# Optimization experiments

Hardware: AMD Instinct MI355X
Metric: run time of the kernel (lower is better)

Reference implementation:

```python
import jax, jax.numpy as jnp
import numpy as np
import math

G = 8        # groups
ORDER = 2    # Taylor order
GAMMA = 1e-4 # RBF gamma
EPS = 1e-5   # GroupNorm eps


def setup_inputs() -> dict:
    key = jax.random.key(0)
    ks = jax.random.split(key, 6)
    B, C_HI, C_LO, P = 16, 512, 512, 256
    H1 = W1 = 64
    H2 = W2 = 32
    s = 0.02
    return {
        "input_high": jax.random.normal(ks[0], (B, C_HI, H1, W1), jnp.float32),
        "input_low": jax.random.normal(ks[1], (B, C_LO, H2, W2), jnp.float32),
        "Wt": jax.random.normal(ks[2], (P, C_HI), jnp.float32) * s,
        "Wp": jax.random.normal(ks[3], (P, C_LO), jnp.float32) * s,
        "Wg": jax.random.normal(ks[4], (P, C_LO), jnp.float32) * s,
        # grouped 1x1 conv planes -> inplanes1: [G, out_per_group, in_per_group]
        "Wz": jax.random.normal(ks[5], (G, C_HI // G, P // G), jnp.float32) * s,
        "gn_w": jnp.ones((C_HI,), jnp.float32),
        "gn_b": jnp.zeros((C_HI,), jnp.float32),
    }


def _taylor_alpha():
    # alpha_k = sqrt((2*gamma)^k / k! * exp(-2*gamma)) for k = 0..ORDER
    ks = np.arange(ORDER + 1)
    fact = np.array([math.factorial(int(k)) for k in ks], dtype=np.float64)
    a = np.sqrt((2.0 * GAMMA) ** ks / fact * np.exp(-2.0 * GAMMA))
    return jnp.asarray(a, jnp.float32)


def reference(input_high, input_low, Wt, Wp, Wg, Wz, gn_w, gn_b):
    # 1x1-conv projections as channel contractions
    t = jnp.einsum('bchw,oc->bohw', input_high, Wt)   # [b, P, h1, w1]
    p = jnp.einsum('bchw,oc->bohw', input_low, Wp)    # [b, P, h2, w2]
    g = jnp.einsum('bchw,oc->bohw', input_low, Wg)    # [b, P, h2, w2]
    b, c1, h1, w1 = t.shape

    alpha = _taylor_alpha()                            # [ORDER+1]
    # split channels into groups, flatten (c/G)*h*w per group
    tg = t.reshape(b, G, -1)                           # [b, G, N1]
    pg = p.reshape(b, G, -1)                           # [b, G, N2]
    gg = g.reshape(b, G, -1)                           # [b, G, N2]

    # low-rank Taylor feature maps: [b, G, ORDER+1, N]
    t_tay = jnp.stack([tg ** k for k in range(ORDER + 1)], axis=2) * alpha[None, None, :, None]
    p_tay = jnp.stack([pg ** k for k in range(ORDER + 1)], axis=2) * alpha[None, None, :, None]

    att = jnp.einsum('bgkn,bgn->bgk', p_tay, gg)       # [b, G, ORDER+1]
    x = jnp.einsum('bgk,bgkn->bgn', att, t_tay)        # [b, G, N1]
    x = x.reshape(b, G, c1 // G, h1, w1)               # grouped feature map

    # grouped 1x1 conv z: planes -> inplanes1
    z = jnp.einsum('bgihw,goi->bgohw', x, Wz)
    z = z.reshape(b, -1, h1, w1)                       # [b, C_HI, h1, w1]

    # GroupNorm(num_groups=G) with affine, then residual
    zg = z.reshape(b, G, -1)
    mu = zg.mean(axis=-1, keepdims=True)
    var = zg.var(axis=-1, keepdims=True)
    zn = ((zg - mu) * jax.lax.rsqrt(var + EPS)).reshape(z.shape)
    out = zn * gn_w[None, :, None, None] + gn_b[None, :, None, None] + input_high
    return out
```

## Files before the change

kernel.cpp:

```cpp
#include <hip/hip_runtime.h>
#include <math.h>

typedef __attribute__((ext_vector_type(8))) short short8;
typedef __attribute__((ext_vector_type(8))) unsigned short u16x8;
typedef __attribute__((ext_vector_type(4))) float f32x4;

#define EPS_ 1e-5f

__device__ inline unsigned int cvtpk(float a, float b) {
    unsigned int r;
    asm("v_cvt_pk_bf16_f32 %0, %1, %2" : "=v"(r) : "v"(a), "v"(b));
    return r;
}

__device__ inline f32x4 mfma16(u16x8 a, u16x8 b, f32x4 c) {
    return __builtin_amdgcn_mfma_f32_16x16x32_bf16((short8)a, (short8)b, c, 0, 0, 0);
}

__global__ __launch_bounds__(256)
void k0s(const float* __restrict__ xlo, float* __restrict__ sxsum)
{
    __shared__ float sred[256];
    int blk = blockIdx.x;
    int cgrp = blk & 15, b = blk >> 4;
    int tid = threadIdx.x;
    int cl = tid >> 3, seg = tid & 7;
    int c = cgrp * 32 + cl;
    const float* row = xlo + ((size_t)b * 512 + c) * 1024 + seg * 128;
    float s = 0.f;
#pragma unroll
    for (int i = 0; i < 32; i++) {
        float4 v = ((const float4*)row)[i];
        s += v.x + v.y + v.z + v.w;
    }
    sred[tid] = s;
    __syncthreads();
    if (seg == 0) {
        float t = 0.f;
#pragma unroll
        for (int e = 0; e < 8; e++) t += sred[cl * 8 + e];
        sxsum[(size_t)b * 512 + c] = t;
    }
}

#define K1_BODY(C0, VCUR, VNXT, DOPREF)                                          \
  {                                                                              \
    if (DOPREF) {                                                                \
        const float* xc = xlo + ((size_t)b * 512 + (C0) + 64 + cs * 8) * 1024 + hw0 + xrow; \
        _Pragma("unroll")                                                        \
        for (int j = 0; j < 8; j++) VNXT[j] = xc[(size_t)j * 1024];              \
    }                                                                            \
    __syncthreads();                                                             \
    _Pragma("unroll")                                                            \
    for (int k = 0; k < 4; k++) {                                                \
        int idx = k * 256 + tid;                                                 \
        int row = idx >> 3, s = idx & 7;                                         \
        const float* pp = Wp + (size_t)(pbase + row) * 512 + (C0) + s * 8;       \
        const float* pg = Wg + (size_t)(pbase + row) * 512 + (C0) + s * 8;       \
        float4 a0 = ((const float4*)pp)[0], a1 = ((const float4*)pp)[1];         \
        float4 b0 = ((const float4*)pg)[0], b1 = ((const float4*)pg)[1];         \
        uint4 qp = { cvtpk(a0.x,a0.y), cvtpk(a0.z,a0.w),                         \
                     cvtpk(a1.x,a1.y), cvtpk(a1.z,a1.w) };                       \
        uint4 qg = { cvtpk(b0.x,b0.y), cvtpk(b0.z,b0.w),                         \
                     cvtpk(b1.x,b1.y), cvtpk(b1.z,b1.w) };                       \
        int off = row * 64 + ((s ^ (row & 7)) << 3);                             \
        *(uint4*)&sWp[off] = qp;                                                 \
        *(uint4*)&sWg[off] = qg;                                                 \
    }                                                                            \
    {                                                                            \
        uint4 q = { cvtpk(VCUR[0],VCUR[1]), cvtpk(VCUR[2],VCUR[3]),              \
                    cvtpk(VCUR[4],VCUR[5]), cvtpk(VCUR[6],VCUR[7]) };            \
        int phys = cs ^ (xrow & 7);                                              \
        *(uint4*)&sX1[xrow * 64 + phys * 8] = q;                                 \
    }                                                                            \
    __syncthreads();                                                             \
    _Pragma("unroll")                                                            \
    for (int kk = 0; kk < 2; kk++) {                                             \
        u16x8 bf[2];                                                             \
        _Pragma("unroll")                                                        \
        for (int ht = 0; ht < 2; ht++) {                                         \
            int row = ht * 16 + l15;                                             \
            bf[ht] = *(const u16x8*)&sX1[row * 64 + (((kk*4+l4) ^ (row&7)) << 3)]; \
        }                                                                        \
        _Pragma("unroll")                                                        \
        for (int i = 0; i < 2; i++) {                                            \
            int row = w * 32 + i * 16 + l15;                                     \
            int off = row * 64 + (((kk*4+l4) ^ (row&7)) << 3);                   \
            u16x8 ap = *(const u16x8*)&sWp[off];                                 \
            u16x8 ag = *(const u16x8*)&sWg[off];                                 \
            _Pragma("unroll")                                                    \
            for (int ht = 0; ht < 2; ht++) {                                     \
                pacc[i][ht] = mfma16(ap, bf[ht], pacc[i][ht]);                   \
                gacc[i][ht] = mfma16(ag, bf[ht], gacc[i][ht]);                   \
            }                                                                    \
        }                                                                        \
    }                                                                            \
  }

__global__ __launch_bounds__(256, 4)
void k1_att(const float* __restrict__ xlo, const float* __restrict__ Wp,
            const float* __restrict__ Wg, float* __restrict__ att_part)
{
    __shared__ unsigned short sWp[8192];
    __shared__ unsigned short sWg[8192];
    __shared__ unsigned short sX1[2048];

    int tid = threadIdx.x;
    int w = tid >> 6, lane = tid & 63;
    int l15 = lane & 15, l4 = lane >> 4;
    int beta = blockIdx.x;
    int tile = beta & 31, mh = (beta >> 5) & 1, b = beta >> 6;
    int hw0 = tile * 32;
    int pbase = mh * 128;
    int xrow = tid & 31, cs = tid >> 5;

    f32x4 pacc[2][2] = {};
    f32x4 gacc[2][2] = {};

    float vbA[8], vbB[8];
    {
        const float* xc = xlo + ((size_t)b * 512 + cs * 8) * 1024 + hw0 + xrow;
#pragma unroll
        for (int j = 0; j < 8; j++) vbA[j] = xc[(size_t)j * 1024];
    }

    for (int kc2 = 0; kc2 < 4; kc2++) {
        int c0 = kc2 * 128;
        K1_BODY(c0,      vbA, vbB, true);
        K1_BODY(c0 + 64, vbB, vbA, (kc2 < 3));
    }

    float s1 = 0.f, s2 = 0.f;
#pragma unroll
    for (int i = 0; i < 2; i++)
#pragma unroll
        for (int ht = 0; ht < 2; ht++)
#pragma unroll
            for (int r = 0; r < 4; r++) {
                float pv = pacc[i][ht][r], gv = gacc[i][ht][r];
                s1 += pv * gv; s2 += pv * pv * gv;
            }
#pragma unroll
    for (int m = 1; m < 64; m <<= 1) {
        s1 += __shfl_xor(s1, m);
        s2 += __shfl_xor(s2, m);
    }
    if (lane == 0) {
        int g = mh * 4 + w;
        float* dst = att_part + ((size_t)(b * 8 + g) * 32 + tile) * 2;
        dst[0] = s1; dst[1] = s2;
    }
}

__global__ __launch_bounds__(64)
void k1b_coef(const float* __restrict__ Wg, const float* __restrict__ sxsum,
              const float* __restrict__ att_part, float* __restrict__ coef,
              float a0s, float a1s, float a2s)
{
    int bg = blockIdx.x;
    int b = bg >> 3, g = bg & 7;
    int l = threadIdx.x;
    float s0 = 0.f;
    for (int cc = 0; cc < 512; cc += 64) {
        int c = cc + l;
        float cs = 0.f;
#pragma unroll
        for (int pp = 0; pp < 32; pp++) cs += Wg[(size_t)(g * 32 + pp) * 512 + c];
        s0 += cs * sxsum[(size_t)b * 512 + c];
    }
    float s1 = (l < 32) ? att_part[((size_t)bg * 32 + l) * 2 + 0] : 0.f;
    float s2 = (l < 32) ? att_part[((size_t)bg * 32 + l) * 2 + 1] : 0.f;
#pragma unroll
    for (int m = 1; m < 64; m <<= 1) {
        s0 += __shfl_xor(s0, m);
        s1 += __shfl_xor(s1, m);
        s2 += __shfl_xor(s2, m);
    }
    if (l == 0) {
        coef[bg * 3 + 0] = a0s * s0;
        coef[bg * 3 + 1] = a1s * s1;
        coef[bg * 3 + 2] = a2s * s2;
    }
}

#define K2_BODY(C0, VCUR, VNXT, DOPREF)                                          \
  {                                                                              \
    if (DOPREF) {                                                                \
        const float* xc = xhi + ((size_t)b * 512 + (C0) + 64 + w * 8) * 4096 + hw0 + xrow; \
        _Pragma("unroll")                                                        \
        for (int j = 0; j < 8; j++) VNXT[j] = xc[(size_t)j * 4096];              \
    }                                                                            \
    __syncthreads();                                                             \
    _Pragma("unroll")                                                            \
    for (int k = 0; k < 4; k++) {                                                \
        int idx = k * 512 + tid;                                                 \
        int row = idx >> 3, s = idx & 7;                                         \
        const float* sp = Wt + (size_t)row * 512 + (C0) + s * 8;                 \
        float4 v0 = ((const float4*)sp)[0];                                      \
        float4 v1 = ((const float4*)sp)[1];                                      \
        uint4 q = { cvtpk(v0.x,v0.y), cvtpk(v0.z,v0.w),                          \
                    cvtpk(v1.x,v1.y), cvtpk(v1.z,v1.w) };                        \
        *(uint4*)&sMain[row * 64 + ((s ^ (row & 7)) << 3)] = q;                  \
    }                                                                            \
    {                                                                            \
        uint4 q = { cvtpk(VCUR[0],VCUR[1]), cvtpk(VCUR[2],VCUR[3]),              \
                    cvtpk(VCUR[4],VCUR[5]), cvtpk(VCUR[6],VCUR[7]) };            \
        int phys = w ^ (xrow & 7);                                               \
        *(uint4*)&sX[xrow * 64 + phys * 8] = q;                                  \
    }                                                                            \
    __syncthreads();                                                             \
    _Pragma("unroll")                                                            \
    for (int kk = 0; kk < 2; kk++) {                                             \
        u16x8 bf[4];                                                             \
        _Pragma("unroll")                                                        \
        for (int ht = 0; ht < 4; ht++) {                                         \
            int row = ht * 16 + l15;                                             \
            bf[ht] = *(const u16x8*)&sX[row * 64 + (((kk*4+l4) ^ (row&7)) << 3)]; \
        }                                                                        \
        _Pragma("unroll")                                                        \
        for (int i = 0; i < 2; i++) {                                            \
            int row = w * 32 + i * 16 + l15;                                     \
            u16x8 af = *(const u16x8*)&sMain[row * 64 + (((kk*4+l4) ^ (row&7)) << 3)]; \
            _Pragma("unroll")                                                    \
            for (int ht = 0; ht < 4; ht++)                                       \
                acc[i][ht] = mfma16(af, bf[ht], acc[i][ht]);                     \
        }                                                                        \
    }                                                                            \
  }

__global__ __launch_bounds__(512, 4)
void k2_main(const float* __restrict__ xhi, const float* __restrict__ Wt,
             const float* __restrict__ Wz, const float* __restrict__ coef,
             float* __restrict__ zout, float* __restrict__ zstat)
{
    __shared__ unsigned short sMain[16384];
    __shared__ unsigned short sX[4096];

    int tid = threadIdx.x;
    int w = tid >> 6, lane = tid & 63;
    int l15 = lane & 15, l4 = lane >> 4;
    int hwt = blockIdx.x & 63, b = blockIdx.x >> 6;
    int hw0 = hwt * 64;
    int xrow = tid & 63;

    const float* cf = coef + (size_t)(b * 8 + w) * 3;
    float c0v = cf[0], c1v = cf[1], c2v = cf[2];

    f32x4 acc[2][4] = {};

    float vbA[8], vbB[8];
    {
        const float* xc = xhi + ((size_t)b * 512 + w * 8) * 4096 + hw0 + xrow;
#pragma unroll
        for (int j = 0; j < 8; j++) vbA[j] = xc[(size_t)j * 4096];
    }

    for (int kc2 = 0; kc2 < 4; kc2++) {
        int c0 = kc2 * 128;
        K2_BODY(c0,      vbA, vbB, true);
        K2_BODY(c0 + 64, vbB, vbA, (kc2 < 3));
    }

#pragma unroll
    for (int i = 0; i < 2; i++)
#pragma unroll
        for (int ht = 0; ht < 4; ht++) {
            f32x4 t = acc[i][ht];
            acc[i][ht] = c1v * t + c2v * t * t;
        }
    __syncthreads();

#pragma unroll
    for (int i = 0; i < 2; i++)
#pragma unroll
        for (int ht = 0; ht < 4; ht++) {
            int row = ht * 16 + l15;
            f32x4 xv = acc[i][ht];
            uint2 q = { cvtpk(xv[0], xv[1]), cvtpk(xv[2], xv[3]) };
            int phys = w * 4 + ((i * 2 + (l4 >> 1)) ^ (row & 3));
            *(uint2*)&sMain[row * 256 + phys * 8 + (l4 & 1) * 4] = q;
        }

    float* sR = (float*)sX;
    {
        const float* wr = Wz + (size_t)tid * 32;
        float s = 0.f;
#pragma unroll
        for (int q = 0; q < 8; q++) {
            float4 v = ((const float4*)wr)[q];
            s += v.x + v.y + v.z + v.w;
        }
        sR[tid] = s;
    }

    u16x8 wzf[4];
#pragma unroll
    for (int ot = 0; ot < 4; ot++) {
        const float* wr = Wz + (size_t)(w * 64 + ot * 16 + l15) * 32 + l4 * 8;
        float4 v0 = ((const float4*)wr)[0];
        float4 v1 = ((const float4*)wr)[1];
        uint4 q = { cvtpk(v0.x,v0.y), cvtpk(v0.z,v0.w),
                    cvtpk(v1.x,v1.y), cvtpk(v1.z,v1.w) };
        wzf[ot] = *(u16x8*)&q;
    }
    __syncthreads();

    float s = 0.f, s2a = 0.f;
    f32x4 zero4 = {0.f, 0.f, 0.f, 0.f};
#pragma unroll
    for (int ht = 0; ht < 4; ht++) {
        int row = ht * 16 + l15;
        u16x8 bfr = *(const u16x8*)&sMain[row * 256 + (w * 4 + (l4 ^ (row & 3))) * 8];
#pragma unroll
        for (int ot = 0; ot < 4; ot++) {
            f32x4 z = mfma16(wzf[ot], bfr, zero4);
            f32x4 rv = *(const f32x4*)&sR[w * 64 + ot * 16 + l4 * 4];
            z = z + c0v * rv;
            float* zp = zout + ((size_t)(b * 512 + w * 64 + ot * 16 + l4 * 4)) * 4096
                      + hw0 + ht * 16 + l15;
#pragma unroll
            for (int r = 0; r < 4; r++) {
                zp[(size_t)r * 4096] = z[r];
                s += z[r]; s2a += z[r] * z[r];
            }
        }
    }
#pragma unroll
    for (int m = 1; m < 64; m <<= 1) {
        s   += __shfl_xor(s, m);
        s2a += __shfl_xor(s2a, m);
    }
    if (lane == 0) {
        atomicAdd(&zstat[(size_t)(b * 8 + w) * 2 + 0], s);
        atomicAdd(&zstat[(size_t)(b * 8 + w) * 2 + 1], s2a);
    }
}

__global__ void k2b_gn(const float* __restrict__ zstat, float* __restrict__ gnstat)
{
    int t = threadIdx.x;
    if (t >= 128) return;
    float S = zstat[t * 2], S2 = zstat[t * 2 + 1];
    const float N = 64.0f * 4096.0f;
    float mean = S / N;
    float var = S2 / N - mean * mean;
    var = var < 0.f ? 0.f : var;
    gnstat[t * 2] = mean;
    gnstat[t * 2 + 1] = rsqrtf(var + EPS_);
}

__global__ __launch_bounds__(256)
void k3_final(float* __restrict__ out, const float* __restrict__ xhi,
              const float* __restrict__ gnstat, const float* __restrict__ gnw,
              const float* __restrict__ gnb)
{
#pragma unroll
    for (int k = 0; k < 4; k++) {
        size_t idx = (size_t)blockIdx.x * 1024 + (size_t)k * 256 + threadIdx.x;
        size_t e = idx * 4;
        int ch = (int)((e >> 12) & 511);
        int b  = (int)(e >> 21);
        int gg = ch >> 6;
        const float* gs = gnstat + (size_t)(b * 8 + gg) * 2;
        float mean = gs[0];
        float w = gnw[ch] * gs[1];
        float bb = gnb[ch];
        float4 z = ((const float4*)out)[idx];
        float4 xv = ((const float4*)xhi)[idx];
        float4 r;
        r.x = (z.x - mean) * w + bb + xv.x;
        r.y = (z.y - mean) * w + bb + xv.y;
        r.z = (z.z - mean) * w + bb + xv.z;
        r.w = (z.w - mean) * w + bb + xv.w;
        ((float4*)out)[idx] = r;
    }
}

extern "C" void kernel_launch(void* const* d_in, const int* in_sizes, int n_in,
                              void* d_out, int out_size, void* d_ws, size_t ws_size,
                              hipStream_t stream) {
    (void)in_sizes; (void)n_in; (void)out_size; (void)ws_size;
    const float* xhi = (const float*)d_in[0];
    const float* xlo = (const float*)d_in[1];
    const float* Wt  = (const float*)d_in[2];
    const float* Wp  = (const float*)d_in[3];
    const float* Wg  = (const float*)d_in[4];
    const float* Wz  = (const float*)d_in[5];
    const float* gnw = (const float*)d_in[6];
    const float* gnb = (const float*)d_in[7];
    float* out = (float*)d_out;
    float* ws  = (float*)d_ws;

    float* sxsum    = ws;
    float* att_part = ws + 8192;
    float* coef     = ws + 16384;
    float* zstat    = ws + 16768;
    float* gnstat   = ws + 17024;

    double g2 = 2.0e-4;
    double ee = exp(-g2);
    float a0s = (float)ee;
    float a1s = (float)(g2 * ee);
    float a2s = (float)(g2 * g2 * 0.5 * ee);

    k0s     <<<dim3(256),  dim3(256), 0, stream>>>(xlo, sxsum);
    k1_att  <<<dim3(1024), dim3(256), 0, stream>>>(xlo, Wp, Wg, att_part);
    k1b_coef<<<dim3(128),  dim3(64),  0, stream>>>(Wg, sxsum, att_part, coef, a0s, a1s, a2s);
    hipMemsetAsync(zstat, 0, 256 * sizeof(float), stream);
    k2_main <<<dim3(1024), dim3(512), 0, stream>>>(xhi, Wt, Wz, coef, out, zstat);
    k2b_gn  <<<dim3(1),    dim3(128), 0, stream>>>(zstat, gnstat);
    k3_final<<<dim3(8192), dim3(256), 0, stream>>>(out, xhi, gnstat, gnw, gnb);
}
```

Baseline: 243.1 us.

## Pre-convert Wt to swizzled bf16 and stream it into LDS via global_load_lds

Adds a small kernel that converts Wt to bf16 once per call, already in the swizzled LDS layout, and stores it in workspace. The main GEMM kernel then copies tiles straight into shared memory with global_load_lds and uses manual waitcnt/barrier control. This removes the per-block fp32 Wt loads and conversions and lets the copy overlap with the x prefetch. It adds an extra launch and a workspace-size dependency, and falls back to the old path when the workspace is too small.

```diff
diff --git a/kernel.cpp b/kernel.cpp
--- a/kernel.cpp
+++ b/kernel.cpp
@@ -15,6 +15,12 @@
 
 __device__ inline f32x4 mfma16(u16x8 a, u16x8 b, f32x4 c) {
     return __builtin_amdgcn_mfma_f32_16x16x32_bf16((short8)a, (short8)b, c, 0, 0, 0);
+}
+
+__device__ inline void gll16(const unsigned short* g, unsigned short* l) {
+    __builtin_amdgcn_global_load_lds(
+        (const __attribute__((address_space(1))) unsigned int*)g,
+        (__attribute__((address_space(3))) unsigned int*)l, 16, 0, 0);
 }
 
 __global__ __launch_bounds__(256)
@@ -41,6 +47,22 @@
         for (int e = 0; e < 8; e++) t += sred[cl * 8 + e];
         sxsum[(size_t)b * 512 + c] = t;
     }
+}
+
+__global__ __launch_bounds__(256)
+void k0w_t(const float* __restrict__ Wt, unsigned short* __restrict__ wtb)
+{
+    int blk = blockIdx.x, tid = threadIdx.x;
+    int kc = blk >> 3, sub = blk & 7;
+    int idx = sub * 256 + tid;
+    int row = idx >> 3, s = idx & 7;
+    int colbase = kc * 64 + ((s ^ (row & 7)) << 3);
+    const float* sp = Wt + (size_t)row * 512 + colbase;
+    float4 v0 = ((const float4*)sp)[0];
+    float4 v1 = ((const float4*)sp)[1];
+    uint4 q = { cvtpk(v0.x, v0.y), cvtpk(v0.z, v0.w),
+                cvtpk(v1.x, v1.y), cvtpk(v1.z, v1.w) };
+    *(uint4*)&wtb[(size_t)(kc * 2048 + idx) * 8] = q;
 }
 
 #define K1_BODY(C0, VCUR, VNXT, DOPREF)                                          \
@@ -183,6 +205,166 @@
     }
 }
 
+#define K2_EPILOGUE                                                              \
+    _Pragma("unroll")                                                            \
+    for (int i = 0; i < 2; i++)                                                  \
+        _Pragma("unroll")                                                        \
+        for (int ht = 0; ht < 4; ht++) {                                         \
+            f32x4 t = acc[i][ht];                                                \
+            acc[i][ht] = c1v * t + c2v * t * t;                                  \
+        }                                                                        \
+    __syncthreads();                                                             \
+    _Pragma("unroll")                                                            \
+    for (int i = 0; i < 2; i++)                                                  \
+        _Pragma("unroll")                                                        \
+        for (int ht = 0; ht < 4; ht++) {                                         \
+            int row = ht * 16 + l15;                                             \
+            f32x4 xv = acc[i][ht];                                               \
+            uint2 q = { cvtpk(xv[0], xv[1]), cvtpk(xv[2], xv[3]) };              \
+            int phys = w * 4 + ((i * 2 + (l4 >> 1)) ^ (row & 3));                \
+            *(uint2*)&sMain[row * 256 + phys * 8 + (l4 & 1) * 4] = q;            \
+        }                                                                        \
+    float* sR = (float*)sX;                                                      \
+    {                                                                            \
+        const float* wr = Wz + (size_t)tid * 32;                                 \
+        float s = 0.f;                                                           \
+        _Pragma("unroll")                                                        \
+        for (int q = 0; q < 8; q++) {                                            \
+            float4 v = ((const float4*)wr)[q];                                   \
+            s += v.x + v.y + v.z + v.w;                                          \
+        }                                                                        \
+        sR[tid] = s;                                                             \
+    }                                                                            \
+    u16x8 wzf[4];                                                                \
+    _Pragma("unroll")                                                            \
+    for (int ot = 0; ot < 4; ot++) {                                             \
+        const float* wr = Wz + (size_t)(w * 64 + ot * 16 + l15) * 32 + l4 * 8;   \
+        float4 v0 = ((const float4*)wr)[0];                                      \
+        float4 v1 = ((const float4*)wr)[1];                                      \
+        uint4 q = { cvtpk(v0.x,v0.y), cvtpk(v0.z,v0.w),                          \
+                    cvtpk(v1.x,v1.y), cvtpk(v1.z,v1.w) };                        \
+        wzf[ot] = *(u16x8*)&q;                                                   \
+    }                                                                            \
+    __syncthreads();                                                             \
+    float s = 0.f, s2a = 0.f;                                                    \
+    f32x4 zero4 = {0.f, 0.f, 0.f, 0.f};                                          \
+    _Pragma("unroll")                                                            \
+    for (int ht = 0; ht < 4; ht++) {                                             \
+        int row = ht * 16 + l15;                                                 \
+        u16x8 bfr = *(const u16x8*)&sMain[row * 256 + (w * 4 + (l4 ^ (row & 3))) * 8]; \
+        _Pragma("unroll")                                                        \
+        for (int ot = 0; ot < 4; ot++) {                                         \
+            f32x4 z = mfma16(wzf[ot], bfr, zero4);                               \
+            f32x4 rv = *(const f32x4*)&sR[w * 64 + ot * 16 + l4 * 4];            \
+            z = z + c0v * rv;                                                    \
+            float* zp = zout + ((size_t)(b * 512 + w * 64 + ot * 16 + l4 * 4)) * 4096 \
+                      + hw0 + ht * 16 + l15;                                     \
+            _Pragma("unroll")                                                    \
+            for (int r = 0; r < 4; r++) {                                        \
+                zp[(size_t)r * 4096] = z[r];                                     \
+                s += z[r]; s2a += z[r] * z[r];                                   \
+            }                                                                    \
+        }                                                                        \
+    }                                                                            \
+    _Pragma("unroll")                                                            \
+    for (int m = 1; m < 64; m <<= 1) {                                           \
+        s   += __shfl_xor(s, m);                                                 \
+        s2a += __shfl_xor(s2a, m);                                               \
+    }                                                                            \
+    if (lane == 0) {                                                             \
+        atomicAdd(&zstat[(size_t)(b * 8 + w) * 2 + 0], s);                       \
+        atomicAdd(&zstat[(size_t)(b * 8 + w) * 2 + 1], s2a);                     \
+    }
+
+#define K2G_BODY(KC, VCUR, VNXT, DOPREF)                                         \
+  {                                                                              \
+                     \
+    asm volatile("s_waitcnt lgkmcnt(0)" ::: "memory");                           \
+    __builtin_amdgcn_s_barrier();                                                \
+    __builtin_amdgcn_sched_barrier(0);                                           \
+       \
+    {                                                                            \
+        uint4 q = { cvtpk(VCUR[0],VCUR[1]), cvtpk(VCUR[2],VCUR[3]),              \
+                    cvtpk(VCUR[4],VCUR[5]), cvtpk(VCUR[6],VCUR[7]) };            \
+        int phys = w ^ (xrow & 7);                                               \
+        *(uint4*)&sX[xrow * 64 + phys * 8] = q;                                  \
+    }                                                                            \
+                  \
+    _Pragma("unroll")                                                            \
+    for (int k = 0; k < 4; k++) {                                                \
+        int u = k * 512 + tid;                                                   \
+        gll16(wtb + (((size_t)(KC) * 2048 + u) << 3), &sMain[u << 3]);           \
+    }                                                                            \
+                     \
+    if (DOPREF) {                                                                \
+        const float* xc = xhi + ((size_t)b * 512 + ((KC) + 1) * 64 + w * 8) * 4096 + hw0 + xrow; \
+        _Pragma("unroll")                                                        \
+        for (int j = 0; j < 8; j++) VNXT[j] = xc[(size_t)j * 4096];              \
+    }                                                                            \
+       \
+    if (DOPREF) { asm volatile("s_waitcnt vmcnt(8) lgkmcnt(0)" ::: "memory"); }  \
+    else        { asm volatile("s_waitcnt vmcnt(0) lgkmcnt(0)" ::: "memory"); }  \
+    __builtin_amdgcn_s_barrier();                                                \
+    __builtin_amdgcn_sched_barrier(0);                                           \
+                                                                 \
+    _Pragma("unroll")                                                            \
+    for (int kk = 0; kk < 2; kk++) {                                             \
+        u16x8 bf[4];                                                             \
+        _Pragma("unroll")                                                        \
+        for (int ht = 0; ht < 4; ht++) {                                         \
+            int row = ht * 16 + l15;                                             \
+            bf[ht] = *(const u16x8*)&sX[row * 64 + (((kk*4+l4) ^ (row&7)) << 3)]; \
+        }                                                                        \
+        _Pragma("unroll")                                                        \
+        for (int i = 0; i < 2; i++) {                                            \
+            int row = w * 32 + i * 16 + l15;                                     \
+            u16x8 af = *(const u16x8*)&sMain[row * 64 + (((kk*4+l4) ^ (row&7)) << 3)]; \
+            _Pragma("unroll")                                                    \
+            for (int ht = 0; ht < 4; ht++)                                       \
+                acc[i][ht] = mfma16(af, bf[ht], acc[i][ht]);                     \
+        }                                                                        \
+    }                                                                            \
+  }
+
+__global__ __launch_bounds__(512, 4)
+void k2_main_g(const float* __restrict__ xhi, const unsigned short* __restrict__ wtb,
+               const float* __restrict__ Wz, const float* __restrict__ coef,
+               float* __restrict__ zout, float* __restrict__ zstat)
+{
+    __shared__ unsigned short sMain[16384];
+    __shared__ unsigned short sX[4096];
+
+    int tid = threadIdx.x;
+    int w = tid >> 6, lane = tid & 63;
+    int l15 = lane & 15, l4 = lane >> 4;
+    int hwt = blockIdx.x & 63, b = blockIdx.x >> 6;
+    int hw0 = hwt * 64;
+    int xrow = tid & 63;
+
+    const float* cf = coef + (size_t)(b * 8 + w) * 3;
+    float c0v = cf[0], c1v = cf[1], c2v = cf[2];
+
+    f32x4 acc[2][4] = {};
+
+    float vbA[8], vbB[8];
+    {
+        const float* xc = xhi + ((size_t)b * 512 + w * 8) * 4096 + hw0 + xrow;
+#pragma unroll
+        for (int j = 0; j < 8; j++) vbA[j] = xc[(size_t)j * 4096];
+    }
+
+    K2G_BODY(0, vbA, vbB, true);
+    K2G_BODY(1, vbB, vbA, true);
+    K2G_BODY(2, vbA, vbB, true);
+    K2G_BODY(3, vbB, vbA, true);
+    K2G_BODY(4, vbA, vbB, true);
+    K2G_BODY(5, vbB, vbA, true);
+    K2G_BODY(6, vbA, vbB, true);
+    K2G_BODY(7, vbB, vbA, false);
+
+    K2_EPILOGUE
+}
+
 #define K2_BODY(C0, VCUR, VNXT, DOPREF)                                          \
   {                                                                              \
     if (DOPREF) {                                                                \
@@ -229,9 +411,9 @@
   }
 
 __global__ __launch_bounds__(512, 4)
-void k2_main(const float* __restrict__ xhi, const float* __restrict__ Wt,
-             const float* __restrict__ Wz, const float* __restrict__ coef,
-             float* __restrict__ zout, float* __restrict__ zstat)
+void k2_main_fb(const float* __restrict__ xhi, const float* __restrict__ Wt,
+                const float* __restrict__ Wz, const float* __restrict__ coef,
+                float* __restrict__ zout, float* __restrict__ zstat)
 {
     __shared__ unsigned short sMain[16384];
     __shared__ unsigned short sX[4096];
@@ -261,79 +443,7 @@
         K2_BODY(c0 + 64, vbB, vbA, (kc2 < 3));
     }
 
-#pragma unroll
-    for (int i = 0; i < 2; i++)
-#pragma unroll
-        for (int ht = 0; ht < 4; ht++) {
-            f32x4 t = acc[i][ht];
-            acc[i][ht] = c1v * t + c2v * t * t;
-        }
-    __syncthreads();
-
-#pragma unroll
-    for (int i = 0; i < 2; i++)
-#pragma unroll
-        for (int ht = 0; ht < 4; ht++) {
-            int row = ht * 16 + l15;
-            f32x4 xv = acc[i][ht];
-            uint2 q = { cvtpk(xv[0], xv[1]), cvtpk(xv[2], xv[3]) };
-            int phys = w * 4 + ((i * 2 + (l4 >> 1)) ^ (row & 3));
-            *(uint2*)&sMain[row * 256 + phys * 8 + (l4 & 1) * 4] = q;
-        }
-
-    float* sR = (float*)sX;
-    {
-        const float* wr = Wz + (size_t)tid * 32;
-        float s = 0.f;
-#pragma unroll
-        for (int q = 0; q < 8; q++) {
-            float4 v = ((const float4*)wr)[q];
-            s += v.x + v.y + v.z + v.w;
-        }
-        sR[tid] = s;
-    }
-
-    u16x8 wzf[4];
-#pragma unroll
-    for (int ot = 0; ot < 4; ot++) {
-        const float* wr = Wz + (size_t)(w * 64 + ot * 16 + l15) * 32 + l4 * 8;
-        float4 v0 = ((const float4*)wr)[0];
-        float4 v1 = ((const float4*)wr)[1];
-        uint4 q = { cvtpk(v0.x,v0.y), cvtpk(v0.z,v0.w),
-                    cvtpk(v1.x,v1.y), cvtpk(v1.z,v1.w) };
-        wzf[ot] = *(u16x8*)&q;
-    }
-    __syncthreads();
-
-    float s = 0.f, s2a = 0.f;
-    f32x4 zero4 = {0.f, 0.f, 0.f, 0.f};
-#pragma unroll
-    for (int ht = 0; ht < 4; ht++) {
-        int row = ht * 16 + l15;
-        u16x8 bfr = *(const u16x8*)&sMain[row * 256 + (w * 4 + (l4 ^ (row & 3))) * 8];
-#pragma unroll
-        for (int ot = 0; ot < 4; ot++) {
-            f32x4 z = mfma16(wzf[ot], bfr, zero4);
-            f32x4 rv = *(const f32x4*)&sR[w * 64 + ot * 16 + l4 * 4];
-            z = z + c0v * rv;
-            float* zp = zout + ((size_t)(b * 512 + w * 64 + ot * 16 + l4 * 4)) * 4096
-                      + hw0 + ht * 16 + l15;
-#pragma unroll
-            for (int r = 0; r < 4; r++) {
-                zp[(size_t)r * 4096] = z[r];
-                s += z[r]; s2a += z[r] * z[r];
-            }
-        }
-    }
-#pragma unroll
-    for (int m = 1; m < 64; m <<= 1) {
-        s   += __shfl_xor(s, m);
-        s2a += __shfl_xor(s2a, m);
-    }
-    if (lane == 0) {
-        atomicAdd(&zstat[(size_t)(b * 8 + w) * 2 + 0], s);
-        atomicAdd(&zstat[(size_t)(b * 8 + w) * 2 + 1], s2a);
-    }
+    K2_EPILOGUE
 }
 
 __global__ void k2b_gn(const float* __restrict__ zstat, float* __restrict__ gnstat)
@@ -379,7 +489,7 @@
 extern "C" void kernel_launch(void* const* d_in, const int* in_sizes, int n_in,
                               void* d_out, int out_size, void* d_ws, size_t ws_size,
                               hipStream_t stream) {
-    (void)in_sizes; (void)n_in; (void)out_size; (void)ws_size;
+    (void)in_sizes; (void)n_in; (void)out_size;
     const float* xhi = (const float*)d_in[0];
     const float* xlo = (const float*)d_in[1];
     const float* Wt  = (const float*)d_in[2];
@@ -396,6 +506,10 @@
     float* coef     = ws + 16384;
     float* zstat    = ws + 16768;
     float* gnstat   = ws + 17024;
+    unsigned short* wtb = (unsigned short*)((char*)d_ws + 69632);
+
+    const size_t WS_NEED = 69632 + 262144;
+    bool use_gll = (ws_size >= WS_NEED);
 
     double g2 = 2.0e-4;
     double ee = exp(-g2);
@@ -407,7 +521,12 @@
     k1_att  <<<dim3(1024), dim3(256), 0, stream>>>(xlo, Wp, Wg, att_part);
     k1b_coef<<<dim3(128),  dim3(64),  0, stream>>>(Wg, sxsum, att_part, coef, a0s, a1s, a2s);
     hipMemsetAsync(zstat, 0, 256 * sizeof(float), stream);
-    k2_main <<<dim3(1024), dim3(512), 0, stream>>>(xhi, Wt, Wz, coef, out, zstat);
+    if (use_gll) {
+        k0w_t    <<<dim3(64),   dim3(256), 0, stream>>>(Wt, wtb);
+        k2_main_g<<<dim3(1024), dim3(512), 0, stream>>>(xhi, wtb, Wz, coef, out, zstat);
+    } else {
+        k2_main_fb<<<dim3(1024), dim3(512), 0, stream>>>(xhi, Wt, Wz, coef, out, zstat);
+    }
     k2b_gn  <<<dim3(1),    dim3(128), 0, stream>>>(zstat, gnstat);
     k3_final<<<dim3(8192), dim3(256), 0, stream>>>(out, xhi, gnstat, gnw, gnb);
 }
```

Result: faster. 212.6 us (-12.5%).
